# Performance work log

Hardware: AMD Instinct MI355X
Metric: run time of the kernel (lower is better)

The kernel has to match this reference:

```python
import jax, jax.numpy as jnp
import numpy as np

MAX_FRAMES = 12
EMBED_DIM = 512
TOPK = 12
NUM_SAMPLES = 500
SIGMA = 0.05
SEL_DIM = 2
NUM_HEADS = 2


def setup_inputs() -> dict:
    key = jax.random.key(0)
    ks = jax.random.split(key, 9)
    D = EMBED_DIM
    C = D // 2
    s = lambda fan_in: 1.0 / np.sqrt(fan_in)
    return {
        "x": jax.random.normal(ks[0], (16, MAX_FRAMES * 50, D), dtype=jnp.float32),
        "ln_g": jnp.ones((D,), jnp.float32),
        "ln_b": jnp.zeros((D,), jnp.float32),
        "w_in": jax.random.normal(ks[1], (D, C), jnp.float32) * s(D),
        "wq": jax.random.normal(ks[2], (C, C), jnp.float32) * s(C),
        "wk": jax.random.normal(ks[3], (C, C), jnp.float32) * s(C),
        "wv": jax.random.normal(ks[4], (C, C), jnp.float32) * s(C),
        "wo": jax.random.normal(ks[5], (C, C), jnp.float32) * s(C),
        "w1": jax.random.normal(ks[6], (2 * C, C), jnp.float32) * s(2 * C),
        "w2": jax.random.normal(ks[7], (C, 1), jnp.float32) * s(C),
    }


def layer_norm(x, g, b, eps=1e-5):
    mu = jnp.mean(x, axis=-1, keepdims=True)
    var = jnp.var(x, axis=-1, keepdims=True)
    return (x - mu) * jax.lax.rsqrt(var + eps) * g + b


def mha(x, wq, wk, wv, wo):
    B, N, C = x.shape
    hd = C // NUM_HEADS
    q = (x @ wq).reshape(B, N, NUM_HEADS, hd).transpose(0, 2, 1, 3)
    k = (x @ wk).reshape(B, N, NUM_HEADS, hd).transpose(0, 2, 1, 3)
    v = (x @ wv).reshape(B, N, NUM_HEADS, hd).transpose(0, 2, 1, 3)
    attn = jax.nn.softmax(jnp.einsum('bhnd,bhmd->bhnm', q, k) / np.sqrt(hd), axis=-1)
    out = jnp.einsum('bhnm,bhmd->bhnd', attn, v).transpose(0, 2, 1, 3).reshape(B, N, C)
    return out @ wo


def predictor(x, ln_g, ln_b, w_in, wq, wk, wv, wo, w1, w2):
    h = jax.nn.gelu(layer_norm(x, ln_g, ln_b) @ w_in, approximate=False)
    h = mha(h, wq, wk, wv, wo)
    B, N, C = h.shape
    g = jnp.mean(h, axis=1, keepdims=True)
    h = jnp.concatenate([h, jnp.broadcast_to(g, (B, N, C))], axis=-1)
    h = jax.nn.gelu(h @ w1, approximate=False)
    return jnp.tanh(h @ w2)  # (B, N, 1)


def perturbed_topk(scores):
    # scores: (b, d) -> soft indicators (b, k, d)
    b, d = scores.shape
    noise = jax.random.normal(jax.random.key(1), (b, NUM_SAMPLES, d), dtype=scores.dtype)
    perturbed = scores[:, None, :] + noise * SIGMA
    _, idx = jax.lax.top_k(perturbed, TOPK)            # (b, ns, k)
    idx = jnp.sort(idx, axis=-1)
    onehot = jax.nn.one_hot(idx, d, dtype=scores.dtype)  # (b, ns, k, d)
    return onehot.mean(axis=1)                          # (b, k, d)


def reference(x, ln_g, ln_b, w_in, wq, wk, wv, wo, w1, w2):
    B, L, D = x.shape
    N = L // MAX_FRAMES
    xf = x.reshape(B * MAX_FRAMES, N, D)
    pred = predictor(xf, ln_g, ln_b, w_in, wq, wk, wv, wo, w1, w2)[..., 0]  # (b, N)
    spatial_score = pred[:, SEL_DIM:]                    # (b, N-2)
    ind = perturbed_topk(spatial_score)                  # (b, k, N-2)
    cls_feat = xf[:, :SEL_DIM, :]
    spatial_feat = xf[:, SEL_DIM:, :]
    sel = jnp.einsum('bkl,bld->bkd', ind, spatial_feat)
    out = jnp.concatenate([cls_feat, sel], axis=1)       # (b, 2+k, D)
    return out.reshape(B, -1, D)
```

## Files before the change

kernel.cpp:

```cpp
#include <hip/hip_runtime.h>
#include <stdint.h>

#define B2      192
#define NTOK    50
#define ROWS    9600
#define D_EMB   512
#define C_DIM   256
#define HD      128
#define NSAMP   500
#define TOPKK   12
#define NSPA    48
#define NSAMP_T 96000
#define NOISE_OFF 61953536ull
#define NOISE_BYTES 18432000ull
#define WS_NEED (NOISE_OFF + NOISE_BYTES)

typedef short short8 __attribute__((ext_vector_type(8)));
typedef float f32x4  __attribute__((ext_vector_type(4)));

__device__ __forceinline__ float gelu_f(float x) {
    return 0.5f * x * (1.0f + erff(x * 0.7071067811865476f));
}
__device__ __forceinline__ uint16_t f2bf(float x) {
    uint32_t u = __float_as_uint(x);
    return (uint16_t)((u + 0x7fffu + ((u >> 16) & 1u)) >> 16);
}
__device__ __forceinline__ float bf2f(uint16_t b) {
    return __uint_as_float(((uint32_t)b) << 16);
}
__device__ __forceinline__ size_t swzA(int m, int k, int K) {
    return ((size_t)(m >> 4) * (K >> 5) + (k >> 5)) * 512
         + (size_t)((((k >> 3) & 3) * 16 + (m & 15)) * 8 + (k & 7));
}

__device__ __forceinline__ uint32_t rotl32(uint32_t x, int r) {
    return (x << r) | (x >> (32 - r));
}
__device__ __forceinline__ void threefry01(uint32_t& x0, uint32_t& x1) {
    const uint32_t ks0 = 0u, ks1 = 1u, ks2 = 0x1BD11BDBu;
    x0 += ks0; x1 += ks1;
#define TFR(r) { x0 += x1; x1 = rotl32(x1, r); x1 ^= x0; }
    TFR(13) TFR(15) TFR(26) TFR(6)  x0 += ks1; x1 += ks2 + 1u;
    TFR(17) TFR(29) TFR(16) TFR(24) x0 += ks2; x1 += ks0 + 2u;
    TFR(13) TFR(15) TFR(26) TFR(6)  x0 += ks0; x1 += ks1 + 3u;
    TFR(17) TFR(29) TFR(16) TFR(24) x0 += ks1; x1 += ks2 + 4u;
    TFR(13) TFR(15) TFR(26) TFR(6)  x0 += ks2; x1 += ks0 + 5u;
#undef TFR
}

__device__ __forceinline__ float erfinv_xla(float x) {
    float w = -log1pf(-x * x);
    float p;
    if (w < 5.0f) {
        w -= 2.5f;
        p = 2.81022636e-08f;
        p = fmaf(p, w, 3.43273939e-07f);
        p = fmaf(p, w, -3.5233877e-06f);
        p = fmaf(p, w, -4.39150654e-06f);
        p = fmaf(p, w, 0.00021858087f);
        p = fmaf(p, w, -0.00125372503f);
        p = fmaf(p, w, -0.00417768164f);
        p = fmaf(p, w, 0.246640727f);
        p = fmaf(p, w, 1.50140941f);
    } else {
        w = sqrtf(w) - 3.0f;
        p = -0.000200214257f;
        p = fmaf(p, w, 0.000100950558f);
        p = fmaf(p, w, 0.00134934322f);
        p = fmaf(p, w, -0.00367342844f);
        p = fmaf(p, w, 0.00573950773f);
        p = fmaf(p, w, -0.0076224613f);
        p = fmaf(p, w, 0.00943887047f);
        p = fmaf(p, w, 1.00167406f);
        p = fmaf(p, w, 2.83297682f);
    }
    return p * x;
}

__device__ __forceinline__ float bits_to_normal(uint32_t bits) {
    float f = __uint_as_float((bits >> 9) | 0x3f800000u) - 1.0f;
    float u = f * 2.0f + (-0.99999994039535522461f);
    u = fmaxf(-0.99999994039535522461f, u);
    return 1.4142135623730951f * erfinv_xla(u);
}

__global__ __launch_bounds__(256) void noise_kernel(float* __restrict__ noise) {
    int T  = blockIdx.x * 256 + threadIdx.x;
    int q  = T / NSAMP_T;
    int g2 = T - q * NSAMP_T;
    uint32_t cbase = (uint32_t)g2 * 48u + (uint32_t)(q * 4);
    float4 o;
    { uint32_t x0=0u, x1=cbase + 0u; threefry01(x0,x1); o.x = bits_to_normal(x0^x1) * 0.05f; }
    { uint32_t x0=0u, x1=cbase + 1u; threefry01(x0,x1); o.y = bits_to_normal(x0^x1) * 0.05f; }
    { uint32_t x0=0u, x1=cbase + 2u; threefry01(x0,x1); o.z = bits_to_normal(x0^x1) * 0.05f; }
    { uint32_t x0=0u, x1=cbase + 3u; threefry01(x0,x1); o.w = bits_to_normal(x0^x1) * 0.05f; }
    ((float4*)noise)[(size_t)q * NSAMP_T + g2] = o;
}

__global__ __launch_bounds__(256) void prep_kernel(const float* __restrict__ x,
                                                   const float* __restrict__ g,
                                                   const float* __restrict__ b,
                                                   short* __restrict__ xh,
                                                   short* __restrict__ xl,
                                                   const float* __restrict__ w_in, const float* __restrict__ wq,
                                                   const float* __restrict__ wk, const float* __restrict__ wv,
                                                   const float* __restrict__ wo, const float* __restrict__ w1,
                                                   short* win_hi, short* win_lo, short* wq_hi, short* wq_lo,
                                                   short* wk_hi, short* wk_lo, short* wv_hi, short* wv_lo,
                                                   short* wo_hi, short* wo_lo, short* w1a_hi, short* w1a_lo) {
    if (blockIdx.x < 2400) {
        int row  = blockIdx.x * 4 + (threadIdx.x >> 6);
        int lane = threadIdx.x & 63;
        const float* rp = x + (size_t)row * D_EMB;
        float4 v0 = *(const float4*)(rp + lane * 8);
        float4 v1 = *(const float4*)(rp + lane * 8 + 4);
        float s  = v0.x + v0.y + v0.z + v0.w + v1.x + v1.y + v1.z + v1.w;
        float s2 = v0.x*v0.x + v0.y*v0.y + v0.z*v0.z + v0.w*v0.w
                 + v1.x*v1.x + v1.y*v1.y + v1.z*v1.z + v1.w*v1.w;
#pragma unroll
        for (int off = 32; off; off >>= 1) {
            s  += __shfl_xor(s,  off);
            s2 += __shfl_xor(s2, off);
        }
        float mu  = s / 512.0f;
        float var = s2 / 512.0f - mu * mu;
        float inv = 1.0f / sqrtf(var + 1e-5f);
        const float* gp = g + lane * 8;
        const float* bp = b + lane * 8;
        float o[8];
        o[0]=(v0.x-mu)*inv*gp[0]+bp[0]; o[1]=(v0.y-mu)*inv*gp[1]+bp[1];
        o[2]=(v0.z-mu)*inv*gp[2]+bp[2]; o[3]=(v0.w-mu)*inv*gp[3]+bp[3];
        o[4]=(v1.x-mu)*inv*gp[4]+bp[4]; o[5]=(v1.y-mu)*inv*gp[5]+bp[5];
        o[6]=(v1.z-mu)*inv*gp[6]+bp[6]; o[7]=(v1.w-mu)*inv*gp[7]+bp[7];
        short8 h8, l8;
#pragma unroll
        for (int j = 0; j < 8; ++j) {
            uint16_t h = f2bf(o[j]);
            h8[j] = (short)h;
            l8[j] = (short)f2bf(o[j] - bf2f(h));
        }
        size_t blk = (size_t)(row >> 4) * 16 + (lane >> 2);
        int inner  = (lane & 3) * 16 + (row & 15);
        ((short8*)xh)[blk * 64 + inner] = h8;
        ((short8*)xl)[blk * 64 + inner] = l8;
    } else {
        int blk = blockIdx.x - 2400;
        const float* W; short *hi, *lo; int K, base;
        if      (blk <  64) { W = w_in; hi = win_hi; lo = win_lo; K = 512; base = 0;   }
        else if (blk <  96) { W = wq;   hi = wq_hi;  lo = wq_lo;  K = 256; base = 64;  }
        else if (blk < 128) { W = wk;   hi = wk_hi;  lo = wk_lo;  K = 256; base = 96;  }
        else if (blk < 160) { W = wv;   hi = wv_hi;  lo = wv_lo;  K = 256; base = 128; }
        else if (blk < 192) { W = wo;   hi = wo_hi;  lo = wo_lo;  K = 256; base = 160; }
        else                { W = w1;   hi = w1a_hi; lo = w1a_lo; K = 256; base = 192; }
        int t = (blk - base) * 256 + threadIdx.x;
        int n = t & 255, k8 = t >> 8;
        short8 h8, l8;
#pragma unroll
        for (int j = 0; j < 8; ++j) {
            float wvl = W[(size_t)(k8 * 8 + j) * 256 + n];
            uint16_t h = f2bf(wvl);
            h8[j] = (short)h;
            l8[j] = (short)f2bf(wvl - bf2f(h));
        }
        size_t bb = (size_t)(n >> 4) * (K >> 5) + (k8 >> 2);
        int inner = (k8 & 3) * 16 + (n & 15);
        ((short8*)hi)[bb * 64 + inner] = h8;
        ((short8*)lo)[bb * 64 + inner] = l8;
    }
}

template<int KB>
__device__ __forceinline__ void mm_core(const short8* __restrict__ pAh, const short8* __restrict__ pAl,
                                        const short8* __restrict__ pBh0, const short8* __restrict__ pBl0,
                                        const short8* __restrict__ pBh1, const short8* __restrict__ pBl1,
                                        f32x4& acc0, f32x4& acc1) {
    short8 ah[3], al[3], bh0[3], bl0[3], bh1[3], bl1[3];
#pragma unroll
    for (int i = 0; i < 2; ++i) {
        int off = i * 64;
        ah[i] = pAh[off];  al[i] = pAl[off];
        bh0[i] = pBh0[off]; bl0[i] = pBl0[off];
        bh1[i] = pBh1[off]; bl1[i] = pBl1[off];
    }
#pragma unroll
    for (int ks = 0; ks < KB; ++ks) {
        int cur = ks % 3;
        if (ks + 2 < KB) {
            int pre = (ks + 2) % 3, off = (ks + 2) * 64;
            ah[pre] = pAh[off];  al[pre] = pAl[off];
            bh0[pre] = pBh0[off]; bl0[pre] = pBl0[off];
            bh1[pre] = pBh1[off]; bl1[pre] = pBl1[off];
        }
        acc0 = __builtin_amdgcn_mfma_f32_16x16x32_bf16(ah[cur], bh0[cur], acc0, 0, 0, 0);
        acc0 = __builtin_amdgcn_mfma_f32_16x16x32_bf16(ah[cur], bl0[cur], acc0, 0, 0, 0);
        acc0 = __builtin_amdgcn_mfma_f32_16x16x32_bf16(al[cur], bh0[cur], acc0, 0, 0, 0);
        acc1 = __builtin_amdgcn_mfma_f32_16x16x32_bf16(ah[cur], bh1[cur], acc1, 0, 0, 0);
        acc1 = __builtin_amdgcn_mfma_f32_16x16x32_bf16(ah[cur], bl1[cur], acc1, 0, 0, 0);
        acc1 = __builtin_amdgcn_mfma_f32_16x16x32_bf16(al[cur], bh1[cur], acc1, 0, 0, 0);
    }
}

__device__ __forceinline__ void epi_store(f32x4 acc, int row0, int col, int N,
                                          float* __restrict__ Cf, short* __restrict__ Chi,
                                          short* __restrict__ Clo,
                                          const float* __restrict__ bias, int act) {
#pragma unroll
    for (int r = 0; r < 4; ++r) {
        int row = row0 + r;
        float v2 = acc[r];
        if (bias) v2 += bias[(size_t)(row / 50) * N + col];
        if (act)  v2 = gelu_f(v2);
        if (Cf) Cf[(size_t)row * N + col] = v2;
        if (Chi) {
            uint16_t h = f2bf(v2);
            size_t ad = swzA(row, col, 256);
            Chi[ad] = (short)h;
            Clo[ad] = (short)f2bf(v2 - bf2f(h));
        }
    }
}

template<int KB>
__global__ __launch_bounds__(256) void gemm_one(const short8* __restrict__ Ah,
                                                const short8* __restrict__ Al,
                                                const short8* __restrict__ Bh,
                                                const short8* __restrict__ Bl,
                                                float* __restrict__ Cf,
                                                short* __restrict__ Chi,
                                                short* __restrict__ Clo,
                                                const float* __restrict__ bias,
                                                int act) {
    int lane = threadIdx.x & 63;
    int wv   = threadIdx.x >> 6;
    int ms   = blockIdx.x * 4 + wv;
    int ns0  = blockIdx.y * 2;
    const short8* pAh  = Ah + (size_t)ms  * KB * 64 + lane;
    const short8* pAl  = Al + (size_t)ms  * KB * 64 + lane;
    const short8* pBh0 = Bh + (size_t)ns0 * KB * 64 + lane;
    const short8* pBl0 = Bl + (size_t)ns0 * KB * 64 + lane;
    const short8* pBh1 = pBh0 + (size_t)KB * 64;
    const short8* pBl1 = pBl0 + (size_t)KB * 64;
    f32x4 acc0 = {0.f,0.f,0.f,0.f}, acc1 = {0.f,0.f,0.f,0.f};
    mm_core<KB>(pAh, pAl, pBh0, pBl0, pBh1, pBl1, acc0, acc1);
    int row0 = ms * 16 + (lane >> 4) * 4;
    int cin  = lane & 15;
    epi_store(acc0, row0, ns0 * 16 + cin,      256, Cf, Chi, Clo, bias, act);
    epi_store(acc1, row0, (ns0 + 1) * 16 + cin, 256, Cf, Chi, Clo, bias, act);
}

__global__ __launch_bounds__(256) void gemm8_pred(const short8* __restrict__ Ah,
                                                  const short8* __restrict__ Al,
                                                  const short8* __restrict__ Bh,
                                                  const short8* __restrict__ Bl,
                                                  const float* __restrict__ gwb,
                                                  const float* __restrict__ w2,
                                                  float* __restrict__ pred_raw) {
    int lane = threadIdx.x & 63;
    int wv   = threadIdx.x >> 6;
    int ms   = blockIdx.x * 4 + wv;
    int ns0  = blockIdx.y * 2;
    const short8* pAh  = Ah + (size_t)ms  * 8 * 64 + lane;
    const short8* pAl  = Al + (size_t)ms  * 8 * 64 + lane;
    const short8* pBh0 = Bh + (size_t)ns0 * 8 * 64 + lane;
    const short8* pBl0 = Bl + (size_t)ns0 * 8 * 64 + lane;
    const short8* pBh1 = pBh0 + 8 * 64;
    const short8* pBl1 = pBl0 + 8 * 64;
    f32x4 acc0 = {0.f,0.f,0.f,0.f}, acc1 = {0.f,0.f,0.f,0.f};
    mm_core<8>(pAh, pAl, pBh0, pBl0, pBh1, pBl1, acc0, acc1);
    int row0 = ms * 16 + (lane >> 4) * 4;
    int cin  = lane & 15;
    int c0   = ns0 * 16 + cin;
    int c1   = (ns0 + 1) * 16 + cin;
    float w2a = w2[c0], w2b = w2[c1];
#pragma unroll
    for (int r = 0; r < 4; ++r) {
        int row = row0 + r;
        int bb  = row / 50;
        float v0 = gelu_f(acc0[r] + gwb[(size_t)bb * 256 + c0]);
        float v1 = gelu_f(acc1[r] + gwb[(size_t)bb * 256 + c1]);
        float t  = v0 * w2a + v1 * w2b;
        t += __shfl_xor(t, 1); t += __shfl_xor(t, 2);
        t += __shfl_xor(t, 4); t += __shfl_xor(t, 8);
        if (cin == 0) atomicAdd(&pred_raw[row], t);
    }
}

__global__ __launch_bounds__(256) void gemm_qkv(const short8* __restrict__ Ah,
                                                const short8* __restrict__ Al,
                                                const short8* __restrict__ Bhq, const short8* __restrict__ Blq,
                                                const short8* __restrict__ Bhk, const short8* __restrict__ Blk,
                                                const short8* __restrict__ Bhv, const short8* __restrict__ Blv,
                                                float* __restrict__ q, float* __restrict__ k,
                                                float* __restrict__ v) {
    int lane = threadIdx.x & 63;
    int wv   = threadIdx.x >> 6;
    int ms   = blockIdx.x * 4 + wv;
    int sel  = blockIdx.y >> 3;
    int ns0  = (blockIdx.y & 7) * 2;
    const short8* Bh = (sel == 0) ? Bhq : (sel == 1) ? Bhk : Bhv;
    const short8* Bl = (sel == 0) ? Blq : (sel == 1) ? Blk : Blv;
    float* C = (sel == 0) ? q : (sel == 1) ? k : v;
    const short8* pAh  = Ah + (size_t)ms  * 8 * 64 + lane;
    const short8* pAl  = Al + (size_t)ms  * 8 * 64 + lane;
    const short8* pBh0 = Bh + (size_t)ns0 * 8 * 64 + lane;
    const short8* pBl0 = Bl + (size_t)ns0 * 8 * 64 + lane;
    const short8* pBh1 = pBh0 + 8 * 64;
    const short8* pBl1 = pBl0 + 8 * 64;
    f32x4 acc0 = {0.f,0.f,0.f,0.f}, acc1 = {0.f,0.f,0.f,0.f};
    mm_core<8>(pAh, pAl, pBh0, pBl0, pBh1, pBl1, acc0, acc1);
    int row0 = ms * 16 + (lane >> 4) * 4;
    int cin  = lane & 15;
    epi_store(acc0, row0, ns0 * 16 + cin,      256, C, nullptr, nullptr, nullptr, 0);
    epi_store(acc1, row0, (ns0 + 1) * 16 + cin, 256, C, nullptr, nullptr, nullptr, 0);
}

__global__ __launch_bounds__(256) void attn_kernel(const float* __restrict__ q,
                                                   const float* __restrict__ k,
                                                   const float* __restrict__ v,
                                                   short* __restrict__ aoh,
                                                   short* __restrict__ aol) {
    __shared__ float sQ[NTOK * 132];
    __shared__ float sK[NTOK * 132];
    __shared__ float sS[NTOK * 51];
    int blk = blockIdx.x;
    int b = blk >> 1, h = blk & 1;
    const size_t base = (size_t)b * NTOK * C_DIM + h * HD;
    int tid = threadIdx.x;
    for (int idx = tid; idx < 1600; idx += 256) {
        int r = idx >> 5, c = (idx & 31) * 4;
        *(float4*)&sQ[r * 132 + c] = *(const float4*)(q + base + (size_t)r * C_DIM + c);
        *(float4*)&sK[r * 132 + c] = *(const float4*)(k + base + (size_t)r * C_DIM + c);
    }
    __syncthreads();
    for (int e = tid; e < 625; e += 256) {
        int i2 = e / 25, j2 = e - i2 * 25;
        int i = i2 * 2, j = j2 * 2;
        const float* qi0 = &sQ[i * 132];
        const float* qi1 = qi0 + 132;
        const float* kj0 = &sK[j * 132];
        const float* kj1 = kj0 + 132;
        float4 a00 = {0,0,0,0}, a01 = {0,0,0,0}, a10 = {0,0,0,0}, a11 = {0,0,0,0};
#pragma unroll
        for (int t = 0; t < 32; ++t) {
            float4 q0 = *(const float4*)&qi0[t * 4];
            float4 q1 = *(const float4*)&qi1[t * 4];
            float4 b0 = *(const float4*)&kj0[t * 4];
            float4 b1 = *(const float4*)&kj1[t * 4];
            a00.x = fmaf(q0.x, b0.x, a00.x); a00.y = fmaf(q0.y, b0.y, a00.y);
            a00.z = fmaf(q0.z, b0.z, a00.z); a00.w = fmaf(q0.w, b0.w, a00.w);
            a01.x = fmaf(q0.x, b1.x, a01.x); a01.y = fmaf(q0.y, b1.y, a01.y);
            a01.z = fmaf(q0.z, b1.z, a01.z); a01.w = fmaf(q0.w, b1.w, a01.w);
            a10.x = fmaf(q1.x, b0.x, a10.x); a10.y = fmaf(q1.y, b0.y, a10.y);
            a10.z = fmaf(q1.z, b0.z, a10.z); a10.w = fmaf(q1.w, b0.w, a10.w);
            a11.x = fmaf(q1.x, b1.x, a11.x); a11.y = fmaf(q1.y, b1.y, a11.y);
            a11.z = fmaf(q1.z, b1.z, a11.z); a11.w = fmaf(q1.w, b1.w, a11.w);
        }
        const float sc = 0.08838834764831845f;
        sS[i * 51 + j]           = (a00.x + a00.y + a00.z + a00.w) * sc;
        sS[i * 51 + j + 1]       = (a01.x + a01.y + a01.z + a01.w) * sc;
        sS[(i + 1) * 51 + j]     = (a10.x + a10.y + a10.z + a10.w) * sc;
        sS[(i + 1) * 51 + j + 1] = (a11.x + a11.y + a11.z + a11.w) * sc;
    }
    __syncthreads();
    for (int idx = tid; idx < 1600; idx += 256) {
        int r = idx >> 5, c = (idx & 31) * 4;
        *(float4*)&sQ[r * 132 + c] = *(const float4*)(v + base + (size_t)r * C_DIM + c);
    }
    if (tid < NTOK) {
        float* row = &sS[tid * 51];
        float m = row[0];
        for (int j = 1; j < NTOK; ++j) m = fmaxf(m, row[j]);
        float sum = 0.f;
        for (int j = 0; j < NTOK; ++j) { float e2 = expf(row[j] - m); row[j] = e2; sum += e2; }
        float inv = 1.0f / sum;
        for (int j = 0; j < NTOK; ++j) row[j] *= inv;
    }
    __syncthreads();
    for (int e = tid; e < 1600; e += 256) {
        int i = e >> 5, d4 = (e & 31) * 4;
        const float* srow = &sS[i * 51];
        float4 acc = {0,0,0,0};
#pragma unroll
        for (int j = 0; j < NTOK; ++j) {
            float w = srow[j];
            float4 v4 = *(const float4*)&sQ[j * 132 + d4];
            acc.x = fmaf(w, v4.x, acc.x); acc.y = fmaf(w, v4.y, acc.y);
            acc.z = fmaf(w, v4.z, acc.z); acc.w = fmaf(w, v4.w, acc.w);
        }
        int row = b * NTOK + i;
        float vals[4] = {acc.x, acc.y, acc.z, acc.w};
#pragma unroll
        for (int c = 0; c < 4; ++c) {
            int col = h * HD + d4 + c;
            uint16_t hh = f2bf(vals[c]);
            size_t ad = swzA(row, col, 256);
            aoh[ad] = (short)hh;
            aol[ad] = (short)f2bf(vals[c] - bf2f(hh));
        }
    }
}

__global__ __launch_bounds__(256) void mean_gw(const float* __restrict__ h2,
                                               const float* __restrict__ w1,
                                               float* __restrict__ gw) {
    __shared__ float sg[C_DIM];
    int b = blockIdx.x, d = threadIdx.x;
    float s = 0.f;
    for (int n = 0; n < NTOK; ++n) s += h2[((size_t)b * NTOK + n) * C_DIM + d];
    sg[d] = s * 0.02f;
    __syncthreads();
    const float* wb = w1 + 256 * 256;
    float acc = 0.f;
#pragma unroll 4
    for (int k = 0; k < C_DIM; ++k)
        acc = fmaf(sg[k], wb[(size_t)k * 256 + d], acc);
    gw[(size_t)b * C_DIM + d] = acc;
}

__device__ __forceinline__ unsigned long long topk_key(uint32_t base, int d,
                                                       const float* __restrict__ sp) {
    uint32_t x0 = 0u, x1 = base + (uint32_t)d;
    threefry01(x0, x1);
    float n  = bits_to_normal(x0 ^ x1);
    float v  = tanhf(sp[d]) + n * 0.05f;
    uint32_t vb   = __float_as_uint(v);
    uint32_t mono = (vb & 0x80000000u) ? ~vb : (vb | 0x80000000u);
    return ((unsigned long long)mono << 6) | (unsigned)(63 - d);
}

#define STEP(li) { unsigned long long mn_ = (key < li) ? key : li; \
                   li = (key > li) ? key : li; key = mn_; }
#define S1  STEP(l0)
#define S2  S1  STEP(l1)
#define S3  S2  STEP(l2)
#define S4  S3  STEP(l3)
#define S5  S4  STEP(l4)
#define S6  S5  STEP(l5)
#define S7  S6  STEP(l6)
#define S8  S7  STEP(l7)
#define S9  S8  STEP(l8)
#define S10 S9  STEP(l9)
#define S11 S10 STEP(l10)
#define S12 S11 STEP(l11)

#define TOPK_MERGE_TAIL                                                        \
    int rowL = p * 64 + lane;                                                  \
    if (hh == 1) {                                                             \
        unsigned long long* r = sK[rowL];                                      \
        r[0]=l0; r[1]=l1; r[2]=l2;  r[3]=l3;  r[4]=l4;   r[5]=l5;              \
        r[6]=l6; r[7]=l7; r[8]=l8;  r[9]=l9;  r[10]=l10; r[11]=l11;            \
    }                                                                          \
    __syncthreads();                                                           \
    if (hh == 0) {                                                             \
        const unsigned long long* r = sK[rowL];                                \
        unsigned long long M0  = (l0  > r[11]) ? l0  : r[11];                  \
        unsigned long long M1  = (l1  > r[10]) ? l1  : r[10];                  \
        unsigned long long M2  = (l2  > r[9])  ? l2  : r[9];                   \
        unsigned long long M3  = (l3  > r[8])  ? l3  : r[8];                   \
        unsigned long long M4  = (l4  > r[7])  ? l4  : r[7];                   \
        unsigned long long M5  = (l5  > r[6])  ? l5  : r[6];                   \
        unsigned long long M6  = (l6  > r[5])  ? l6  : r[5];                   \
        unsigned long long M7  = (l7  > r[4])  ? l7  : r[4];                   \
        unsigned long long M8  = (l8  > r[3])  ? l8  : r[3];                   \
        unsigned long long M9  = (l9  > r[2])  ? l9  : r[2];                   \
        unsigned long long M10 = (l10 > r[1])  ? l10 : r[1];                   \
        unsigned long long M11 = (l11 > r[0])  ? l11 : r[0];                   \
        unsigned long long m = 0ull;                                           \
        m |= 1ull << (unsigned)(M0  & 63ull);  m |= 1ull << (unsigned)(M1  & 63ull); \
        m |= 1ull << (unsigned)(M2  & 63ull);  m |= 1ull << (unsigned)(M3  & 63ull); \
        m |= 1ull << (unsigned)(M4  & 63ull);  m |= 1ull << (unsigned)(M5  & 63ull); \
        m |= 1ull << (unsigned)(M6  & 63ull);  m |= 1ull << (unsigned)(M7  & 63ull); \
        m |= 1ull << (unsigned)(M8  & 63ull);  m |= 1ull << (unsigned)(M9  & 63ull); \
        m |= 1ull << (unsigned)(M10 & 63ull);  m |= 1ull << (unsigned)(M11 & 63ull); \
        EMIT(M0)  EMIT(M1)  EMIT(M2)  EMIT(M3)  EMIT(M4)  EMIT(M5)             \
        EMIT(M6)  EMIT(M7)  EMIT(M8)  EMIT(M9)  EMIT(M10) EMIT(M11)            \
    }
#define EMIT(Mi) { unsigned a_ = (unsigned)(Mi & 63ull); \
                   int kpos_ = 11 - __popcll(m & ((1ull << a_) - 1ull)); \
                   int d_ = 63 - (int)a_; \
                   atomicAdd(&counts[((size_t)b * TOPKK + kpos_) * NSPA + d_], 1); }

__global__ __launch_bounds__(256, 4) void topk_noise(const float* __restrict__ pred,
                                                     const float4* __restrict__ nz4,
                                                     int* __restrict__ counts) {
    __shared__ unsigned long long sK[128][13];
    __shared__ float sSP[2][48];
    int lane = threadIdx.x & 63;
    int wv   = threadIdx.x >> 6;
    int p    = wv >> 1;
    int hh   = wv & 1;
    int b0   = (blockIdx.x * 128) / NSAMP;
    if (threadIdx.x < 96) {
        int r = threadIdx.x / 48, dd = threadIdx.x - r * 48;
        int bb = b0 + r; if (bb > B2 - 1) bb = B2 - 1;
        sSP[r][dd] = tanhf(pred[bb * NTOK + 2 + dd]);
    }
    int g = blockIdx.x * 128 + p * 64 + lane;
    int b = g / NSAMP;
    int bo = b - b0;
    __syncthreads();
    const float* spl = &sSP[bo][hh * 24];
    const float4* nq = nz4 + (size_t)(hh * 6) * NSAMP_T + g;

    float4 n0 = nq[0 * NSAMP_T], n1 = nq[1 * NSAMP_T], n2 = nq[2 * NSAMP_T];
    float4 n3 = nq[3 * NSAMP_T], n4 = nq[4 * NSAMP_T], n5 = nq[5 * NSAMP_T];

    unsigned long long l0=0ull,l1=0ull,l2=0ull,l3=0ull,l4=0ull,l5=0ull,
                       l6=0ull,l7=0ull,l8=0ull,l9=0ull,l10=0ull,l11=0ull;
    unsigned long long key;

#define MKKEY(dd, nv) { float v_ = spl[dd] + (nv); uint32_t vb_ = __float_as_uint(v_); \
    uint32_t mono_ = (vb_ & 0x80000000u) ? ~vb_ : (vb_ | 0x80000000u); \
    key = ((unsigned long long)mono_ << 6) | (unsigned)(63 - (hh * 24 + (dd))); }

    MKKEY(0,  n0.x) S1   MKKEY(1,  n0.y) S2   MKKEY(2,  n0.z) S3   MKKEY(3,  n0.w) S4
    MKKEY(4,  n1.x) S5   MKKEY(5,  n1.y) S6   MKKEY(6,  n1.z) S7   MKKEY(7,  n1.w) S8
    MKKEY(8,  n2.x) S9   MKKEY(9,  n2.y) S10  MKKEY(10, n2.z) S11  MKKEY(11, n2.w) S12
    MKKEY(12, n3.x) S12  MKKEY(13, n3.y) S12  MKKEY(14, n3.z) S12  MKKEY(15, n3.w) S12
    MKKEY(16, n4.x) S12  MKKEY(17, n4.y) S12  MKKEY(18, n4.z) S12  MKKEY(19, n4.w) S12
    MKKEY(20, n5.x) S12  MKKEY(21, n5.y) S12  MKKEY(22, n5.z) S12  MKKEY(23, n5.w) S12
#undef MKKEY

    TOPK_MERGE_TAIL
}

__global__ __launch_bounds__(256, 4) void topk_fb(const float* __restrict__ pred,
                                                  int* __restrict__ counts) {
    __shared__ unsigned long long sK[128][13];
    int lane = threadIdx.x & 63;
    int wv   = threadIdx.x >> 6;
    int p    = wv >> 1;
    int hh   = wv & 1;
    int g    = blockIdx.x * 128 + p * 64 + lane;
    int b    = g / NSAMP;
    int s    = g - b * NSAMP;
    uint32_t base = (uint32_t)((b * NSAMP + s) * NSPA);
    const float* sp = pred + b * NTOK + 2;
    int d0 = hh * 24;

    unsigned long long l0=0ull,l1=0ull,l2=0ull,l3=0ull,l4=0ull,l5=0ull,
                       l6=0ull,l7=0ull,l8=0ull,l9=0ull,l10=0ull,l11=0ull;
    unsigned long long key;

    key = topk_key(base, d0 + 0,  sp); S1
    key = topk_key(base, d0 + 1,  sp); S2
    key = topk_key(base, d0 + 2,  sp); S3
    key = topk_key(base, d0 + 3,  sp); S4
    key = topk_key(base, d0 + 4,  sp); S5
    key = topk_key(base, d0 + 5,  sp); S6
    key = topk_key(base, d0 + 6,  sp); S7
    key = topk_key(base, d0 + 7,  sp); S8
    key = topk_key(base, d0 + 8,  sp); S9
    key = topk_key(base, d0 + 9,  sp); S10
    key = topk_key(base, d0 + 10, sp); S11
    key = topk_key(base, d0 + 11, sp); S12
#pragma unroll 2
    for (int dd = 12; dd < 24; ++dd) {
        key = topk_key(base, d0 + dd, sp); S12
    }

    TOPK_MERGE_TAIL
}
#undef EMIT
#undef TOPK_MERGE_TAIL
#undef STEP
#undef S1
#undef S2
#undef S3
#undef S4
#undef S5
#undef S6
#undef S7
#undef S8
#undef S9
#undef S10
#undef S11
#undef S12

__global__ __launch_bounds__(256) void select_out2(const float* __restrict__ x,
                                                   const int* __restrict__ counts,
                                                   float* __restrict__ out) {
    int b = blockIdx.x;
    int d = threadIdx.x;
    __shared__ float sw[TOPKK * NSPA];
    __shared__ int anyl[NSPA];
    for (int i = d; i < TOPKK * NSPA; i += 256)
        sw[i] = (float)counts[(size_t)b * TOPKK * NSPA + i] * 0.002f;
    __syncthreads();
    if (d < NSPA) {
        int a = 0;
        for (int k2 = 0; k2 < TOPKK; ++k2) a |= (sw[k2 * NSPA + d] != 0.0f);
        anyl[d] = a;
    }
    __syncthreads();
    {
        const float* xr0 = x + (size_t)(b * NTOK) * D_EMB;
        out[(size_t)(b * 14 + 0) * D_EMB + d]       = xr0[d];
        out[(size_t)(b * 14 + 0) * D_EMB + d + 256] = xr0[d + 256];
        out[(size_t)(b * 14 + 1) * D_EMB + d]       = xr0[D_EMB + d];
        out[(size_t)(b * 14 + 1) * D_EMB + d + 256] = xr0[D_EMB + d + 256];
    }
    float a0[TOPKK], a1[TOPKK];
#pragma unroll
    for (int k2 = 0; k2 < TOPKK; ++k2) { a0[k2] = 0.f; a1[k2] = 0.f; }
    for (int l = 0; l < NSPA; ++l) {
        if (!anyl[l]) continue;
        const float* xr = x + (size_t)(b * NTOK + 2 + l) * D_EMB;
        float v0 = xr[d], v1 = xr[d + 256];
#pragma unroll
        for (int k2 = 0; k2 < TOPKK; ++k2) {
            float w = sw[k2 * NSPA + l];
            a0[k2] = fmaf(w, v0, a0[k2]);
            a1[k2] = fmaf(w, v1, a1[k2]);
        }
    }
#pragma unroll
    for (int k2 = 0; k2 < TOPKK; ++k2) {
        out[(size_t)(b * 14 + 2 + k2) * D_EMB + d]       = a0[k2];
        out[(size_t)(b * 14 + 2 + k2) * D_EMB + d + 256] = a1[k2];
    }
}

extern "C" void kernel_launch(void* const* d_in, const int* in_sizes, int n_in,
                              void* d_out, int out_size, void* d_ws, size_t ws_size,
                              hipStream_t stream) {
    const float* x    = (const float*)d_in[0];
    const float* ln_g = (const float*)d_in[1];
    const float* ln_b = (const float*)d_in[2];
    const float* w_in = (const float*)d_in[3];
    const float* wq   = (const float*)d_in[4];
    const float* wk   = (const float*)d_in[5];
    const float* wv   = (const float*)d_in[6];
    const float* wo   = (const float*)d_in[7];
    const float* w1   = (const float*)d_in[8];
    const float* w2   = (const float*)d_in[9];
    float* out = (float*)d_out;

    char* W = (char*)d_ws;
    short* xn_hi  = (short*)(W + 0);
    short* xn_lo  = (short*)(W + 9830400);
    short* ao_hi  = (short*)(W + 0);
    short* ao_lo  = (short*)(W + 4915200);
    short* h2_hi  = (short*)(W + 9830400);
    short* h2_lo  = (short*)(W + 14745600);
    short* h1_hi  = (short*)(W + 19660800);
    short* h1_lo  = (short*)(W + 24576000);
    float* q      = (float*)(W + 29491200);
    float* h2f    = (float*)(W + 29491200);
    float* k      = (float*)(W + 39321600);
    float* v      = (float*)(W + 49152000);
    short* win_hi = (short*)(W + 58982400);
    short* win_lo = (short*)(W + 59244544);
    short* wq_hi  = (short*)(W + 59506688);
    short* wq_lo  = (short*)(W + 59637760);
    short* wk_hi  = (short*)(W + 59768832);
    short* wk_lo  = (short*)(W + 59899904);
    short* wv_hi  = (short*)(W + 60030976);
    short* wv_lo  = (short*)(W + 60162048);
    short* wo_hi  = (short*)(W + 60293120);
    short* wo_lo  = (short*)(W + 60424192);
    short* w1a_hi = (short*)(W + 60555264);
    short* w1a_lo = (short*)(W + 60686336);
    float* gw     = (float*)(W + 61276160);
    float* pred   = (float*)(W + 61472768);
    int*   counts = (int*)  (W + 61511168);
    float* noise  = (float*)(W + NOISE_OFF);

    const bool nzmode = ws_size >= WS_NEED;

    hipMemsetAsync(W + 61472768, 0, 38400 + (size_t)B2 * TOPKK * NSPA * sizeof(int), stream);
    if (nzmode) noise_kernel<<<4500, 256, 0, stream>>>(noise);
    prep_kernel<<<2624, 256, 0, stream>>>(x, ln_g, ln_b, xn_hi, xn_lo,
        w_in, wq, wk, wv, wo, w1,
        win_hi, win_lo, wq_hi, wq_lo, wk_hi, wk_lo, wv_hi, wv_lo,
        wo_hi, wo_lo, w1a_hi, w1a_lo);
    gemm_one<16><<<dim3(150, 8), 256, 0, stream>>>((const short8*)xn_hi, (const short8*)xn_lo,
        (const short8*)win_hi, (const short8*)win_lo, nullptr, h1_hi, h1_lo, nullptr, 1);
    gemm_qkv<<<dim3(150, 24), 256, 0, stream>>>((const short8*)h1_hi, (const short8*)h1_lo,
        (const short8*)wq_hi, (const short8*)wq_lo, (const short8*)wk_hi, (const short8*)wk_lo,
        (const short8*)wv_hi, (const short8*)wv_lo, q, k, v);
    attn_kernel<<<B2 * 2, 256, 0, stream>>>(q, k, v, ao_hi, ao_lo);
    gemm_one<8><<<dim3(150, 8), 256, 0, stream>>>((const short8*)ao_hi, (const short8*)ao_lo,
        (const short8*)wo_hi, (const short8*)wo_lo, h2f, h2_hi, h2_lo, nullptr, 0);
    mean_gw<<<B2, 256, 0, stream>>>(h2f, w1, gw);
    gemm8_pred<<<dim3(150, 8), 256, 0, stream>>>((const short8*)h2_hi, (const short8*)h2_lo,
        (const short8*)w1a_hi, (const short8*)w1a_lo, gw, w2, pred);
    if (nzmode) topk_noise<<<750, 256, 0, stream>>>(pred, (const float4*)noise, counts);
    else        topk_fb<<<750, 256, 0, stream>>>(pred, counts);
    select_out2<<<B2, 256, 0, stream>>>(x, counts, out);
}
```

Baseline: 303.7 us.

## Retile attention kernel with 4x4 register blocking, swizzled LDS and wave softmax

The attention kernel now stores Q/K/V in shared memory with an XOR-swizzled 128-float row layout in place of padded rows. The QK^T stage gives each thread a 4x4 output tile (169 threads) and the PV stage gives each thread 4 rows, so each LDS load is reused across more FMAs. Softmax is parallelised across wavefronts with shuffle reductions in place of one thread per row. The risks are that only 169 of 256 threads do QK^T work and that the larger accumulator tiles raise register pressure. This is one kernel among several in the pipeline.

```diff
diff --git a/kernel.cpp b/kernel.cpp
--- a/kernel.cpp
+++ b/kernel.cpp
@@ -314,91 +314,127 @@
     epi_store(acc1, row0, (ns0 + 1) * 16 + cin, 256, C, nullptr, nullptr, nullptr, 0);
 }
 
+#define ASLOT(r, s) ((r) * 128 + (((s) ^ (((r) >> 2) & 7)) << 2))
 __global__ __launch_bounds__(256) void attn_kernel(const float* __restrict__ q,
                                                    const float* __restrict__ k,
                                                    const float* __restrict__ v,
                                                    short* __restrict__ aoh,
                                                    short* __restrict__ aol) {
-    __shared__ float sQ[NTOK * 132];
-    __shared__ float sK[NTOK * 132];
+    __shared__ float sQ[NTOK * 128];
+    __shared__ float sK[NTOK * 128];
     __shared__ float sS[NTOK * 51];
     int blk = blockIdx.x;
     int b = blk >> 1, h = blk & 1;
     const size_t base = (size_t)b * NTOK * C_DIM + h * HD;
     int tid = threadIdx.x;
     for (int idx = tid; idx < 1600; idx += 256) {
-        int r = idx >> 5, c = (idx & 31) * 4;
-        *(float4*)&sQ[r * 132 + c] = *(const float4*)(q + base + (size_t)r * C_DIM + c);
-        *(float4*)&sK[r * 132 + c] = *(const float4*)(k + base + (size_t)r * C_DIM + c);
+        int r = idx >> 5, s = idx & 31;
+        int ps = ASLOT(r, s);
+        *(float4*)&sQ[ps] = *(const float4*)(q + base + (size_t)r * C_DIM + s * 4);
+        *(float4*)&sK[ps] = *(const float4*)(k + base + (size_t)r * C_DIM + s * 4);
     }
     __syncthreads();
-    for (int e = tid; e < 625; e += 256) {
-        int i2 = e / 25, j2 = e - i2 * 25;
-        int i = i2 * 2, j = j2 * 2;
-        const float* qi0 = &sQ[i * 132];
-        const float* qi1 = qi0 + 132;
-        const float* kj0 = &sK[j * 132];
-        const float* kj1 = kj0 + 132;
-        float4 a00 = {0,0,0,0}, a01 = {0,0,0,0}, a10 = {0,0,0,0}, a11 = {0,0,0,0};
-#pragma unroll
+    if (tid < 169) {
+        int i2 = tid / 13, j2 = tid - i2 * 13;
+        int i0 = i2 * 4, j0 = j2 * 4;
+        int kq = i2 & 7, kk = j2 & 7;
+        const float* qp[4];
+        const float* kp[4];
+#pragma unroll
+        for (int r = 0; r < 4; ++r) {
+            int ir = i0 + r; if (ir > 49) ir = 49;
+            int jr = j0 + r; if (jr > 49) jr = 49;
+            qp[r] = &sQ[ir * 128];
+            kp[r] = &sK[jr * 128];
+        }
+        f32x4 acc[4][4];
+#pragma unroll
+        for (int r = 0; r < 4; ++r)
+#pragma unroll
+            for (int c = 0; c < 4; ++c) acc[r][c] = (f32x4){0.f, 0.f, 0.f, 0.f};
+#pragma unroll 4
         for (int t = 0; t < 32; ++t) {
-            float4 q0 = *(const float4*)&qi0[t * 4];
-            float4 q1 = *(const float4*)&qi1[t * 4];
-            float4 b0 = *(const float4*)&kj0[t * 4];
-            float4 b1 = *(const float4*)&kj1[t * 4];
-            a00.x = fmaf(q0.x, b0.x, a00.x); a00.y = fmaf(q0.y, b0.y, a00.y);
-            a00.z = fmaf(q0.z, b0.z, a00.z); a00.w = fmaf(q0.w, b0.w, a00.w);
-            a01.x = fmaf(q0.x, b1.x, a01.x); a01.y = fmaf(q0.y, b1.y, a01.y);
-            a01.z = fmaf(q0.z, b1.z, a01.z); a01.w = fmaf(q0.w, b1.w, a01.w);
-            a10.x = fmaf(q1.x, b0.x, a10.x); a10.y = fmaf(q1.y, b0.y, a10.y);
-            a10.z = fmaf(q1.z, b0.z, a10.z); a10.w = fmaf(q1.w, b0.w, a10.w);
-            a11.x = fmaf(q1.x, b1.x, a11.x); a11.y = fmaf(q1.y, b1.y, a11.y);
-            a11.z = fmaf(q1.z, b1.z, a11.z); a11.w = fmaf(q1.w, b1.w, a11.w);
+            int oq = (t ^ kq) << 2, ok = (t ^ kk) << 2;
+            f32x4 qr[4], kr[4];
+#pragma unroll
+            for (int r = 0; r < 4; ++r) qr[r] = *(const f32x4*)(qp[r] + oq);
+#pragma unroll
+            for (int c = 0; c < 4; ++c) kr[c] = *(const f32x4*)(kp[c] + ok);
+#pragma unroll
+            for (int r = 0; r < 4; ++r)
+#pragma unroll
+                for (int c = 0; c < 4; ++c) acc[r][c] += qr[r] * kr[c];
         }
         const float sc = 0.08838834764831845f;
-        sS[i * 51 + j]           = (a00.x + a00.y + a00.z + a00.w) * sc;
-        sS[i * 51 + j + 1]       = (a01.x + a01.y + a01.z + a01.w) * sc;
-        sS[(i + 1) * 51 + j]     = (a10.x + a10.y + a10.z + a10.w) * sc;
-        sS[(i + 1) * 51 + j + 1] = (a11.x + a11.y + a11.z + a11.w) * sc;
+#pragma unroll
+        for (int r = 0; r < 4; ++r) {
+            if (i0 + r < 50) {
+#pragma unroll
+                for (int c = 0; c < 4; ++c) {
+                    if (j0 + c < 50) {
+                        f32x4 a = acc[r][c];
+                        sS[(i0 + r) * 51 + (j0 + c)] = (a[0] + a[1] + a[2] + a[3]) * sc;
+                    }
+                }
+            }
+        }
     }
     __syncthreads();
     for (int idx = tid; idx < 1600; idx += 256) {
-        int r = idx >> 5, c = (idx & 31) * 4;
-        *(float4*)&sQ[r * 132 + c] = *(const float4*)(v + base + (size_t)r * C_DIM + c);
-    }
-    if (tid < NTOK) {
-        float* row = &sS[tid * 51];
-        float m = row[0];
-        for (int j = 1; j < NTOK; ++j) m = fmaxf(m, row[j]);
-        float sum = 0.f;
-        for (int j = 0; j < NTOK; ++j) { float e2 = expf(row[j] - m); row[j] = e2; sum += e2; }
-        float inv = 1.0f / sum;
-        for (int j = 0; j < NTOK; ++j) row[j] *= inv;
+        int r = idx >> 5, s = idx & 31;
+        *(float4*)&sQ[ASLOT(r, s)] = *(const float4*)(v + base + (size_t)r * C_DIM + s * 4);
+    }
+    {
+        int wid = tid >> 6, lane = tid & 63;
+        for (int i = wid; i < NTOK; i += 4) {
+            float val = (lane < NTOK) ? sS[i * 51 + lane] : -3.0e38f;
+            float m = val;
+#pragma unroll
+            for (int off = 32; off; off >>= 1) m = fmaxf(m, __shfl_xor(m, off));
+            float e2 = expf(val - m);
+            float s = e2;
+#pragma unroll
+            for (int off = 32; off; off >>= 1) s += __shfl_xor(s, off);
+            if (lane < NTOK) sS[i * 51 + lane] = e2 * (1.0f / s);
+        }
     }
     __syncthreads();
-    for (int e = tid; e < 1600; e += 256) {
-        int i = e >> 5, d4 = (e & 31) * 4;
-        const float* srow = &sS[i * 51];
-        float4 acc = {0,0,0,0};
-#pragma unroll
+    for (int e = tid; e < 416; e += 256) {
+        int i2 = e >> 5;
+        int s4 = e & 31;
+        int i0 = i2 * 4;
+        const float* sr[4];
+#pragma unroll
+        for (int r = 0; r < 4; ++r) {
+            int ir = i0 + r; if (ir > 49) ir = 49;
+            sr[r] = &sS[ir * 51];
+        }
+        f32x4 acc[4];
+#pragma unroll
+        for (int r = 0; r < 4; ++r) acc[r] = (f32x4){0.f, 0.f, 0.f, 0.f};
         for (int j = 0; j < NTOK; ++j) {
-            float w = srow[j];
-            float4 v4 = *(const float4*)&sQ[j * 132 + d4];
-            acc.x = fmaf(w, v4.x, acc.x); acc.y = fmaf(w, v4.y, acc.y);
-            acc.z = fmaf(w, v4.z, acc.z); acc.w = fmaf(w, v4.w, acc.w);
-        }
-        int row = b * NTOK + i;
-        float vals[4] = {acc.x, acc.y, acc.z, acc.w};
-#pragma unroll
-        for (int c = 0; c < 4; ++c) {
-            int col = h * HD + d4 + c;
-            uint16_t hh = f2bf(vals[c]);
-            size_t ad = swzA(row, col, 256);
-            aoh[ad] = (short)hh;
-            aol[ad] = (short)f2bf(vals[c] - bf2f(hh));
-        }
-    }
-}
+            f32x4 v4 = *(const f32x4*)&sQ[ASLOT(j, s4)];
+#pragma unroll
+            for (int r = 0; r < 4; ++r) acc[r] += v4 * sr[r][j];
+        }
+#pragma unroll
+        for (int r = 0; r < 4; ++r) {
+            if (i0 + r < 50) {
+                int row = b * NTOK + i0 + r;
+#pragma unroll
+                for (int c = 0; c < 4; ++c) {
+                    int col = h * HD + s4 * 4 + c;
+                    float val = acc[r][c];
+                    uint16_t hh2 = f2bf(val);
+                    size_t ad = swzA(row, col, 256);
+                    aoh[ad] = (short)hh2;
+                    aol[ad] = (short)f2bf(val - bf2f(hh2));
+                }
+            }
+        }
+    }
+}
+#undef ASLOT
 
 __global__ __launch_bounds__(256) void mean_gw(const float* __restrict__ h2,
                                                const float* __restrict__ w1,
```

New measurement: 299.0 us. No clear change (-1.6%).
